# Performance work log

Hardware: AMD Instinct MI355X
Metric: run time of the kernel (lower is better)

Reference implementation:

```python
import jax, jax.numpy as jnp
import numpy as np
import math

N = 20000          # nodes (residues)
E = 640000         # edges
CS = 384           # c_s
CZ = 128           # c_z
CH = 16            # c_hidden
H = 8              # no_heads
PQK = 8            # no_qk_points == no_v_points (forced equal, see notes)
FS = 128           # scalar channels in feat_irreps
PIN = 16           # vector channels in feat_irreps
HC = H * CH        # 128
HPQ = H * PQK * 3  # 192
CZ4 = CZ // 4      # 32
OUT_IN = HC + 3 * H + H + H * CZ4  # 416 actual concat width
INF = 100000.0
EPS = 1e-8


def setup_inputs() -> dict:
    key = jax.random.key(0)
    ks = jax.random.split(key, 16)
    w = lambda k, i, o: (jax.random.normal(k, (i, o), jnp.float32) / np.float32(np.sqrt(i)))
    frame_s = jax.random.normal(ks[0], (N, CS), jnp.float32)
    tfn_t = jax.random.normal(ks[1], (N, FS + 3 * PIN), jnp.float32)
    z = jax.random.normal(ks[2], (E, CZ), jnp.float32)
    edge_index = jax.random.randint(ks[3], (2, E), 0, N)
    mask = jnp.ones((N,), jnp.float32)
    # Rigid transforms: proper-ish rotations via QR, translations
    rot, _ = jnp.linalg.qr(jax.random.normal(ks[4], (N, 3, 3), jnp.float32))
    trans = jax.random.normal(ks[5], (N, 3), jnp.float32)
    return {
        "frame_s": frame_s, "tfn_t": tfn_t, "z": z,
        "edge_index": edge_index, "mask": mask,
        "rot": rot, "trans": trans,
        "Wq": w(ks[6], CS, HC), "bq": jnp.zeros((HC,), jnp.float32),
        "Wk_s": w(ks[7], FS, HC), "Wk_v": w(ks[8], PIN, PQK),
        "Wqp": w(ks[9], CS, HPQ), "bqp": jnp.zeros((HPQ,), jnp.float32),
        "Wb": w(ks[10], CZ, H), "bb": jnp.zeros((H,), jnp.float32),
        "Wdz": w(ks[11], CZ, CZ4), "bdz": jnp.zeros((CZ4,), jnp.float32),
        # ipa_point_weights_init_: softplus(hw) == 1  =>  hw = log(e - 1)
        "head_weights": jnp.full((H,), np.float32(np.log(np.e - 1.0))),
        "Wout": w(ks[12], OUT_IN, CS), "bout": jnp.zeros((CS,), jnp.float32),
    }


def _segment_softmax(a, seg, n):
    # pyg-style numerically stable segment softmax over edges grouped by seg
    m = jax.ops.segment_max(a, seg, num_segments=n)
    m = jnp.where(jnp.isfinite(m), m, 0.0)
    e = jnp.exp(a - m[seg])
    s = jax.ops.segment_sum(e, seg, num_segments=n)
    return e / (s[seg] + 1e-16)


def _forward(frame_s, tfn_t, z, mask, rot, trans,
             Wq, bq, Wk_s, Wk_v, Wqp, bqp, Wb, bb, Wdz, bdz,
             head_weights, Wout, bout, edge_index):
    n = frame_s.shape[0]
    src = edge_index[1]
    dst = edge_index[0]

    # scalar queries: [N,H,C]
    q = (frame_s @ Wq + bq).reshape(n, H, CH)

    # o3.Linear (feat_irreps -> k_irreps): scalars mix scalars, vectors mix vectors.
    # NOTE: original code uses linear_k for BOTH k and v (faithful bug), so v==k.
    scal = tfn_t[:, :FS]
    vecs = tfn_t[:, FS:].reshape(n, PIN, 3)
    k_scal = scal @ Wk_s                                   # [N, HC]
    k_vec = jnp.einsum('npx,pq->nqx', vecs, Wk_v)          # [N, PQK, 3]
    k = k_scal.reshape(n, H, CH)
    v = k
    k_tail = k_vec.reshape(n, PQK * 3)                     # [N, 24]
    # torch: split([3]*PQK) then stack(dim=-1) -> [N,3,PQK], then view [N,H,-1,3]
    k_pts = jnp.stack(jnp.split(k_tail, PQK, axis=-1), axis=-1)  # [N,3,PQK]
    k_pts = k_pts.reshape(n, H, -1, 3)                     # [N,H,1,3]
    v_pts = k_pts

    # query points, rigid-transformed: [N,H,PQK,3]
    q_pts = frame_s @ Wqp + bqp                            # [N, 3*H*PQK]
    q_pts = jnp.stack(jnp.split(q_pts, 3, axis=-1), axis=-1)  # [N, H*PQK, 3]
    q_pts = jnp.einsum('nij,npj->npi', rot, q_pts) + trans[:, None, :]
    q_pts = q_pts.reshape(n, H, PQK, 3)

    # scalar attention logits [E,H]
    a = jnp.einsum('ehc,ehc->eh', q[src], k[dst])
    a = a * np.float32(math.sqrt(1.0 / (3 * CH)))
    b = z @ Wb + bb                                        # [E,H]
    a = a + np.float32(math.sqrt(1.0 / 3)) * b

    # point attention: disp [E,H,PQK,3] (k_pts broadcasts over points)
    disp = q_pts[src] - k_pts[dst]
    pt_att = jnp.sum(disp * disp, axis=-1)                 # [E,H,PQK]
    hw = jax.nn.softplus(head_weights) * np.float32(math.sqrt(1.0 / (3 * (PQK * 9.0 / 2))))
    pt_att = -0.5 * jnp.sum(pt_att * hw[None, :, None], axis=-1)  # [E,H]

    edge_mask = INF * (mask[dst] * mask[src] - 1.0)        # [E]
    a = a + pt_att + edge_mask[:, None]

    a = _segment_softmax(a, src, n)                        # [E,H]

    # scalar output
    o = jax.ops.segment_sum(a[..., None] * v[dst], src, num_segments=n)  # [N,H,C]
    o = o.reshape(n, HC)

    # point output
    o_pt = jax.ops.segment_sum(a[:, :, None, None] * v_pts[dst], src, num_segments=n)  # [N,H,1,3]
    o_pt = jnp.einsum('nji,nhpj->nhpi', rot, o_pt - trans[:, None, None, :])  # invert_apply
    o_pt_norm = jnp.sqrt(jnp.sum(o_pt * o_pt, axis=-1) + EPS).reshape(n, H)
    o_pt = o_pt.reshape(n, -1, 3)                          # [N,H,3]

    # pair output
    pair_z = z @ Wdz + bdz                                 # [E,CZ4]
    o_pair = jax.ops.segment_sum(a[..., None] * pair_z[:, None, :], src, num_segments=n)  # [N,H,CZ4]
    o_pair = o_pair.reshape(n, H * CZ4)

    feats = jnp.concatenate(
        [o, o_pt[..., 0], o_pt[..., 1], o_pt[..., 2], o_pt_norm, o_pair], axis=-1)  # [N,416]
    return feats @ Wout + bout                             # [N, CS]


def reference(frame_s, tfn_t, z, edge_index, mask, rot, trans,
              Wq, bq, Wk_s, Wk_v, Wqp, bqp, Wb, bb, Wdz, bdz,
              head_weights, Wout, bout):
    return _forward(frame_s, tfn_t, z, mask, rot, trans,
                    Wq, bq, Wk_s, Wk_v, Wqp, bqp, Wb, bb, Wdz, bdz,
                    head_weights, Wout, bout, edge_index)
```

## Files before the change

### kernel.cpp

```cpp
#include <hip/hip_runtime.h>
#include <math.h>

typedef __attribute__((ext_vector_type(8))) short short8;
typedef __attribute__((ext_vector_type(4))) float f32x4;

static __device__ inline unsigned short f2bf(float f) {
    union { float f; unsigned u; } v; v.f = f;
    unsigned r = v.u + 0x7FFF + ((v.u >> 16) & 1);
    return (unsigned short)(r >> 16);
}

template<int WJ>
__global__ __launch_bounds__(256) void gemm_mfma(
    const float* __restrict__ A, int lda,
    const float* __restrict__ BT, int ldb,
    const float* __restrict__ bias,
    float* __restrict__ C, int ldc,
    int M, int N, int K)
{
    constexpr int GBN = WJ * 32;
    __shared__ unsigned short As[128 * 72];
    __shared__ unsigned short Bs[GBN * 72];

    const int t = threadIdx.x;
    const int wid = t >> 6, lane = t & 63;
    const int wm = (wid & 1) * 64;
    const int wn = (wid >> 1) * (WJ * 16);
    const int row16 = lane & 15, quad = lane >> 4;
    const int bm = blockIdx.x * 128;
    const int bn = blockIdx.y * GBN;

    f32x4 acc[4][WJ];
    #pragma unroll
    for (int i = 0; i < 4; ++i)
        #pragma unroll
        for (int j = 0; j < WJ; ++j)
            #pragma unroll
            for (int r = 0; r < 4; ++r) acc[i][j][r] = 0.f;

    const int ktiles = (K + 63) >> 6;
    for (int kt = 0; kt < ktiles; ++kt) {
        const int k0 = kt << 6;
        #pragma unroll
        for (int it = 0; it < 8; ++it) {
            int f = it * 256 + t;
            int row = f >> 4, kq = (f & 15) << 2;
            float4 av = make_float4(0.f, 0.f, 0.f, 0.f);
            if (bm + row < M && k0 + kq < K)
                av = *(const float4*)(A + (size_t)(bm + row) * lda + k0 + kq);
            ushort4 uv;
            uv.x = f2bf(av.x); uv.y = f2bf(av.y); uv.z = f2bf(av.z); uv.w = f2bf(av.w);
            *(ushort4*)(&As[row * 72 + kq]) = uv;
        }
        #pragma unroll
        for (int it = 0; it < WJ * 2; ++it) {
            int f = it * 256 + t;
            int row = f >> 4, kq = (f & 15) << 2;
            float4 bv = make_float4(0.f, 0.f, 0.f, 0.f);
            if (bn + row < N && k0 + kq < K)
                bv = *(const float4*)(BT + (size_t)(bn + row) * ldb + k0 + kq);
            ushort4 uv;
            uv.x = f2bf(bv.x); uv.y = f2bf(bv.y); uv.z = f2bf(bv.z); uv.w = f2bf(bv.w);
            *(ushort4*)(&Bs[row * 72 + kq]) = uv;
        }
        __syncthreads();

        #pragma unroll
        for (int ks = 0; ks < 64; ks += 32) {
            short8 af[4], bfv[WJ];
            #pragma unroll
            for (int i = 0; i < 4; ++i)
                af[i] = *(const short8*)(&As[(wm + i * 16 + row16) * 72 + ks + quad * 8]);
            #pragma unroll
            for (int j = 0; j < WJ; ++j)
                bfv[j] = *(const short8*)(&Bs[(wn + j * 16 + row16) * 72 + ks + quad * 8]);
            #pragma unroll
            for (int i = 0; i < 4; ++i)
                #pragma unroll
                for (int j = 0; j < WJ; ++j)
                    acc[i][j] = __builtin_amdgcn_mfma_f32_16x16x32_bf16(af[i], bfv[j], acc[i][j], 0, 0, 0);
        }
        __syncthreads();
    }

    #pragma unroll
    for (int i = 0; i < 4; ++i)
        #pragma unroll
        for (int j = 0; j < WJ; ++j) {
            int col = bn + wn + j * 16 + row16;
            if (col >= N) continue;
            float bv = bias ? bias[col] : 0.f;
            #pragma unroll
            for (int r = 0; r < 4; ++r) {
                int row = bm + wm + i * 16 + quad * 4 + r;
                if (row < M) C[(size_t)row * ldc + col] = acc[i][j][r] + bv;
            }
        }
}

__global__ void prep_kernel(const float* __restrict__ Wq, const float* __restrict__ bq,
                            const float* __restrict__ Wqp, const float* __restrict__ bqp,
                            const float* __restrict__ Wb, const float* __restrict__ bb,
                            const float* __restrict__ Wdz, const float* __restrict__ bdz,
                            const float* __restrict__ Wks, const float* __restrict__ Wout,
                            float* __restrict__ wqqpT, float* __restrict__ bqqp,
                            float* __restrict__ wcatT, float* __restrict__ bcat,
                            float* __restrict__ wksT, float* __restrict__ woutT)
{
    int gid = blockIdx.x * 256 + threadIdx.x;
    int stride = gridDim.x * 256;
    for (int i = gid; i < 320 * 384; i += stride) {
        int o = i / 384, c = i % 384;
        wqqpT[i] = (o < 128) ? Wq[c * 128 + o] : Wqp[c * 192 + (o - 128)];
    }
    for (int i = gid; i < 320; i += stride) bqqp[i] = (i < 128) ? bq[i] : bqp[i - 128];
    for (int i = gid; i < 40 * 128; i += stride) {
        int o = i >> 7, c = i & 127;
        wcatT[i] = (o < 8) ? Wb[c * 8 + o] : Wdz[c * 32 + (o - 8)];
    }
    for (int i = gid; i < 40; i += stride) bcat[i] = (i < 8) ? bb[i] : bdz[i - 8];
    for (int i = gid; i < 128 * 128; i += stride) {
        int o = i >> 7, c = i & 127;
        wksT[i] = Wks[c * 128 + o];
    }
    for (int i = gid; i < 384 * 416; i += stride) {
        int o = i / 416, c = i % 416;
        woutT[i] = Wout[c * 384 + o];
    }
}

__global__ void kpts_kernel(const float* __restrict__ tfn, const float* __restrict__ Wkv,
                            float* __restrict__ kpts, int n)
{
    int t = blockIdx.x * 256 + threadIdx.x;
    if (t >= n * 24) return;
    int node = t / 24, f = t % 24;
    int a = f >> 3;
    int b = f & 7;
    const float* vr = tfn + (size_t)node * 176 + 128;
    float s = 0.f;
    #pragma unroll
    for (int p = 0; p < 16; ++p) s += vr[p * 3 + a] * Wkv[p * 8 + b];
    kpts[t] = s;
}

__global__ void qpts_kernel(const float* __restrict__ qpraw, const float* __restrict__ rot,
                            const float* __restrict__ trans, float* __restrict__ qpts, int n)
{
    int t = blockIdx.x * 256 + threadIdx.x;
    if (t >= n * 64) return;
    int node = t / 64, hk = t % 64;
    const float* qr = qpraw + (size_t)node * 320;
    float r0 = qr[hk], r1 = qr[64 + hk], r2 = qr[128 + hk];
    const float* R = rot + (size_t)node * 9;
    const float* T = trans + (size_t)node * 3;
    float* o = qpts + (size_t)node * 192 + hk * 3;
    #pragma unroll
    for (int i = 0; i < 3; ++i)
        o[i] = R[i * 3 + 0] * r0 + R[i * 3 + 1] * r1 + R[i * 3 + 2] * r2 + T[i];
}

__global__ void count_kernel(const int* __restrict__ srcA, int* __restrict__ cnt, int E)
{
    int e = blockIdx.x * 256 + threadIdx.x;
    if (e < E) atomicAdd(&cnt[srcA[e]], 1);
}

__global__ void scan_kernel(const int* __restrict__ cnt, int* __restrict__ off,
                            int* __restrict__ cur, int n)
{
    __shared__ int sums[1024];
    int t = threadIdx.x;
    int chunk = (n + 1023) >> 10;
    int begin = t * chunk;
    int local = 0;
    for (int j = 0; j < chunk; ++j) {
        int i = begin + j;
        if (i < n) local += cnt[i];
    }
    sums[t] = local;
    __syncthreads();
    for (int d = 1; d < 1024; d <<= 1) {
        int x = sums[t];
        int y = (t >= d) ? sums[t - d] : 0;
        __syncthreads();
        sums[t] = x + y;
        __syncthreads();
    }
    int run = sums[t] - local;
    for (int j = 0; j < chunk; ++j) {
        int i = begin + j;
        if (i < n) {
            off[i] = run;
            cur[i] = run;
            run += cnt[i];
        }
    }
}

__global__ void fill_kernel(const int* __restrict__ srcA, int* __restrict__ cur,
                            int* __restrict__ elist, int E)
{
    int e = blockIdx.x * 256 + threadIdx.x;
    if (e < E) {
        int s = srcA[e];
        int pos = atomicAdd(&cur[s], 1);
        elist[pos] = e;
    }
}

__global__ __launch_bounds__(256) void attn_kernel(
    const int* __restrict__ dstA,
    const int* __restrict__ off, const int* __restrict__ cnt, const int* __restrict__ elist,
    const float* __restrict__ qqp, const float* __restrict__ kbuf,
    const float* __restrict__ qpts, const float* __restrict__ kpts,
    const float* __restrict__ bpair, const float* __restrict__ mask,
    const float* __restrict__ hwin,
    const float* __restrict__ rot, const float* __restrict__ trans,
    float* __restrict__ feats, int n)
{
    int wave = threadIdx.x >> 6;
    int lane = threadIdx.x & 63;
    int s = blockIdx.x * 4 + wave;
    if (s >= n) return;
    int es = lane >> 3;
    int h  = lane & 7;

    float qh[16];
    {
        const float* qp = qqp + (size_t)s * 320 + h * 16;
        #pragma unroll
        for (int c = 0; c < 16; ++c) qh[c] = qp[c];
    }
    float qpt[24];
    {
        const float* pp = qpts + (size_t)s * 192 + h * 24;
        #pragma unroll
        for (int j = 0; j < 24; ++j) qpt[j] = pp[j];
    }
    float hwv = log1pf(__expf(hwin[h])) * 0.09622504486493764f;
    float mask_s = mask[s];
    int myoff = off[s], mycnt = cnt[s];

    float ssum = 0.f;
    float oacc[16];
    #pragma unroll
    for (int c = 0; c < 16; ++c) oacc[c] = 0.f;
    float optacc[3] = {0.f, 0.f, 0.f};
    float opacc[8][4];
    #pragma unroll
    for (int j = 0; j < 8; ++j)
        #pragma unroll
        for (int c = 0; c < 4; ++c) opacc[j][c] = 0.f;

    int nb = (mycnt + 7) >> 3;
    for (int b = 0; b < nb; ++b) {
        int idx = b * 8 + es;
        bool valid = idx < mycnt;
        int e = valid ? elist[myoff + idx] : 0;
        int d = dstA[e];

        const float* kr = kbuf + (size_t)d * 128 + h * 16;
        float4 ka = *(const float4*)(kr + 0);
        float4 kb = *(const float4*)(kr + 4);
        float4 kc = *(const float4*)(kr + 8);
        float4 kd = *(const float4*)(kr + 12);

        const float* kp = kpts + (size_t)d * 24 + h * 3;
        float kp0 = kp[0], kp1 = kp[1], kp2 = kp[2];

        const float* bp = bpair + (size_t)e * 40;
        float bh = bp[h];
        float4 pair4 = *(const float4*)(bp + 8 + h * 4);

        float qk = qh[0] * ka.x + qh[1] * ka.y + qh[2] * ka.z + qh[3] * ka.w
                 + qh[4] * kb.x + qh[5] * kb.y + qh[6] * kb.z + qh[7] * kb.w
                 + qh[8] * kc.x + qh[9] * kc.y + qh[10] * kc.z + qh[11] * kc.w
                 + qh[12] * kd.x + qh[13] * kd.y + qh[14] * kd.z + qh[15] * kd.w;

        float pt = 0.f;
        #pragma unroll
        for (int pp = 0; pp < 8; ++pp) {
            float d0 = qpt[pp * 3 + 0] - kp0;
            float d1 = qpt[pp * 3 + 1] - kp1;
            float d2 = qpt[pp * 3 + 2] - kp2;
            pt += d0 * d0 + d1 * d1 + d2 * d2;
        }

        float md = mask[d];
        float logit = 0.14433756729740643f * qk
                    + 0.5773502691896258f * bh
                    - 0.5f * hwv * pt
                    + 100000.0f * (mask_s * md - 1.0f);
        float w = valid ? __expf(logit) : 0.f;

        ssum += w;
        oacc[0] += w * ka.x; oacc[1] += w * ka.y; oacc[2] += w * ka.z; oacc[3] += w * ka.w;
        oacc[4] += w * kb.x; oacc[5] += w * kb.y; oacc[6] += w * kb.z; oacc[7] += w * kb.w;
        oacc[8] += w * kc.x; oacc[9] += w * kc.y; oacc[10] += w * kc.z; oacc[11] += w * kc.w;
        oacc[12] += w * kd.x; oacc[13] += w * kd.y; oacc[14] += w * kd.z; oacc[15] += w * kd.w;
        optacc[0] += w * kp0;
        optacc[1] += w * kp1;
        optacc[2] += w * kp2;

        #pragma unroll
        for (int jh = 0; jh < 8; ++jh) {
            float wj = __shfl(w, (es << 3) + jh);
            opacc[jh][0] += wj * pair4.x;
            opacc[jh][1] += wj * pair4.y;
            opacc[jh][2] += wj * pair4.z;
            opacc[jh][3] += wj * pair4.w;
        }
    }

    #pragma unroll
    for (int delta = 8; delta <= 32; delta <<= 1) {
        ssum += __shfl_xor(ssum, delta);
        #pragma unroll
        for (int c = 0; c < 16; ++c) oacc[c] += __shfl_xor(oacc[c], delta);
        #pragma unroll
        for (int i = 0; i < 3; ++i) optacc[i] += __shfl_xor(optacc[i], delta);
        #pragma unroll
        for (int j = 0; j < 8; ++j)
            #pragma unroll
            for (int c = 0; c < 4; ++c) opacc[j][c] += __shfl_xor(opacc[j][c], delta);
    }

    float invj[8];
    #pragma unroll
    for (int jh = 0; jh < 8; ++jh)
        invj[jh] = 1.f / (__shfl(ssum, jh) + 1e-16f);

    if (es == 0) {
        float inv = 1.f / (ssum + 1e-16f);
        float* f = feats + (size_t)s * 416;
        #pragma unroll
        for (int c = 0; c < 16; c += 4) {
            float4 v = make_float4(oacc[c] * inv, oacc[c + 1] * inv, oacc[c + 2] * inv, oacc[c + 3] * inv);
            *(float4*)(&f[h * 16 + c]) = v;
        }
        const float* T = trans + (size_t)s * 3;
        const float* R = rot + (size_t)s * 9;
        float v0 = optacc[0] * inv - T[0];
        float v1 = optacc[1] * inv - T[1];
        float v2 = optacc[2] * inv - T[2];
        float r0 = R[0] * v0 + R[3] * v1 + R[6] * v2;
        float r1 = R[1] * v0 + R[4] * v1 + R[7] * v2;
        float r2 = R[2] * v0 + R[5] * v1 + R[8] * v2;
        f[128 + h] = r0;
        f[136 + h] = r1;
        f[144 + h] = r2;
        f[152 + h] = sqrtf(r0 * r0 + r1 * r1 + r2 * r2 + 1e-8f);
        #pragma unroll
        for (int jh = 0; jh < 8; ++jh) {
            float4 v = make_float4(opacc[jh][0] * invj[jh], opacc[jh][1] * invj[jh],
                                   opacc[jh][2] * invj[jh], opacc[jh][3] * invj[jh]);
            *(float4*)(&f[160 + jh * 32 + h * 4]) = v;
        }
    }
}

extern "C" void kernel_launch(void* const* d_in, const int* in_sizes, int n_in,
                              void* d_out, int out_size, void* d_ws, size_t ws_size,
                              hipStream_t stream)
{
    const float* frame_s = (const float*)d_in[0];
    const float* tfn     = (const float*)d_in[1];
    const float* z       = (const float*)d_in[2];
    const int*   ei      = (const int*)d_in[3];
    const float* mask    = (const float*)d_in[4];
    const float* rot     = (const float*)d_in[5];
    const float* trans   = (const float*)d_in[6];
    const float* Wq      = (const float*)d_in[7];
    const float* bq      = (const float*)d_in[8];
    const float* Wks     = (const float*)d_in[9];
    const float* Wkv     = (const float*)d_in[10];
    const float* Wqp     = (const float*)d_in[11];
    const float* bqp     = (const float*)d_in[12];
    const float* Wb      = (const float*)d_in[13];
    const float* bb      = (const float*)d_in[14];
    const float* Wdz     = (const float*)d_in[15];
    const float* bdz     = (const float*)d_in[16];
    const float* hw      = (const float*)d_in[17];
    const float* Wout    = (const float*)d_in[18];
    const float* bout    = (const float*)d_in[19];
    float* out = (float*)d_out;

    int n = in_sizes[0] / 384;
    int E = in_sizes[3] / 2;
    const int* dstA = ei;
    const int* srcA = ei + E;

    float* ws = (float*)d_ws;
    size_t p = 0;
    auto alloc = [&](size_t elems) -> float* {
        float* r = ws + p;
        p += (elems + 15) & ~((size_t)15);
        return r;
    };
    float* qqpbuf = alloc((size_t)n * 320);
    float* qpts   = alloc((size_t)n * 192);
    float* kbuf   = alloc((size_t)n * 128);
    float* kpts   = alloc((size_t)n * 24);
    float* feats  = alloc((size_t)n * 416);
    float* bpair  = alloc((size_t)E * 40);
    float* wqqpT  = alloc(320 * 384);
    float* bqqp   = alloc(320);
    float* wcatT  = alloc(40 * 128);
    float* bcat   = alloc(64);
    float* wksT   = alloc(128 * 128);
    float* woutT  = alloc(384 * 416);
    int* cnt   = (int*)alloc((size_t)n);
    int* off   = (int*)alloc((size_t)n);
    int* cur   = (int*)alloc((size_t)n);
    int* elist = (int*)alloc((size_t)E);

    hipMemsetAsync(cnt, 0, (size_t)n * sizeof(int), stream);
    prep_kernel<<<512, 256, 0, stream>>>(Wq, bq, Wqp, bqp, Wb, bb, Wdz, bdz, Wks, Wout,
                                         wqqpT, bqqp, wcatT, bcat, wksT, woutT);

    count_kernel<<<(E + 255) / 256, 256, 0, stream>>>(srcA, cnt, E);
    scan_kernel<<<1, 1024, 0, stream>>>(cnt, off, cur, n);
    fill_kernel<<<(E + 255) / 256, 256, 0, stream>>>(srcA, cur, elist, E);

    {
        dim3 g((n + 127) / 128, (320 + 127) / 128);
        gemm_mfma<4><<<g, 256, 0, stream>>>(frame_s, 384, wqqpT, 384, bqqp, qqpbuf, 320, n, 320, 384);
    }
    {
        dim3 g((n + 127) / 128, 1);
        gemm_mfma<4><<<g, 256, 0, stream>>>(tfn, 176, wksT, 128, nullptr, kbuf, 128, n, 128, 128);
    }
    {
        dim3 g((E + 127) / 128, 1);
        gemm_mfma<2><<<g, 256, 0, stream>>>(z, 128, wcatT, 128, bcat, bpair, 40, E, 40, 128);
    }
    kpts_kernel<<<(n * 24 + 255) / 256, 256, 0, stream>>>(tfn, Wkv, kpts, n);
    qpts_kernel<<<(n * 64 + 255) / 256, 256, 0, stream>>>(qqpbuf + 128, rot, trans, qpts, n);

    attn_kernel<<<(n + 3) / 4, 256, 0, stream>>>(dstA, off, cnt, elist,
                                                 qqpbuf, kbuf, qpts, kpts, bpair, mask, hw,
                                                 rot, trans, feats, n);

    {
        dim3 g((n + 127) / 128, (384 + 127) / 128);
        gemm_mfma<4><<<g, 256, 0, stream>>>(feats, 416, woutT, 416, bout, out, 384, n, 384, 416);
    }
    (void)n_in; (void)out_size; (void)ws_size;
}
```

Baseline: 905.6 us.

## Gather edge GEMM into CSR order, fold logit scales into weights, widen GEMM tiles

Measured after the change: 966.7 us. 1.07x slower.

```diff
diff --git a/kernel.cpp b/kernel.cpp
--- a/kernel.cpp
+++ b/kernel.cpp
@@ -10,9 +10,10 @@
     return (unsigned short)(r >> 16);
 }
 
-template<int WJ>
+template<int WJ, bool GATHER>
 __global__ __launch_bounds__(256) void gemm_mfma(
     const float* __restrict__ A, int lda,
+    const int* __restrict__ gidx,
     const float* __restrict__ BT, int ldb,
     const float* __restrict__ bias,
     float* __restrict__ C, int ldc,
@@ -46,8 +47,12 @@
             int f = it * 256 + t;
             int row = f >> 4, kq = (f & 15) << 2;
             float4 av = make_float4(0.f, 0.f, 0.f, 0.f);
-            if (bm + row < M && k0 + kq < K)
-                av = *(const float4*)(A + (size_t)(bm + row) * lda + k0 + kq);
+            if (bm + row < M && k0 + kq < K) {
+                size_t ar;
+                if constexpr (GATHER) ar = (size_t)gidx[bm + row];
+                else                  ar = (size_t)(bm + row);
+                av = *(const float4*)(A + ar * lda + k0 + kq);
+            }
             ushort4 uv;
             uv.x = f2bf(av.x); uv.y = f2bf(av.y); uv.z = f2bf(av.z); uv.w = f2bf(av.w);
             *(ushort4*)(&As[row * 72 + kq]) = uv;
@@ -105,20 +110,24 @@
                             const float* __restrict__ Wks, const float* __restrict__ Wout,
                             float* __restrict__ wqqpT, float* __restrict__ bqqp,
                             float* __restrict__ wcatT, float* __restrict__ bcat,
-                            float* __restrict__ wksT, float* __restrict__ woutT)
-{
+                            float* __restrict__ wksT, float* __restrict__ woutT,
+                            int* __restrict__ cnt, int n)
+{
+    const float SC_QK = 0.14433756729740643f;
+    const float SC_B  = 0.5773502691896258f;
     int gid = blockIdx.x * 256 + threadIdx.x;
     int stride = gridDim.x * 256;
+    for (int i = gid; i < n; i += stride) cnt[i] = 0;
     for (int i = gid; i < 320 * 384; i += stride) {
         int o = i / 384, c = i % 384;
-        wqqpT[i] = (o < 128) ? Wq[c * 128 + o] : Wqp[c * 192 + (o - 128)];
-    }
-    for (int i = gid; i < 320; i += stride) bqqp[i] = (i < 128) ? bq[i] : bqp[i - 128];
+        wqqpT[i] = (o < 128) ? Wq[c * 128 + o] * SC_QK : Wqp[c * 192 + (o - 128)];
+    }
+    for (int i = gid; i < 320; i += stride) bqqp[i] = (i < 128) ? bq[i] * SC_QK : bqp[i - 128];
     for (int i = gid; i < 40 * 128; i += stride) {
         int o = i >> 7, c = i & 127;
-        wcatT[i] = (o < 8) ? Wb[c * 8 + o] : Wdz[c * 32 + (o - 8)];
-    }
-    for (int i = gid; i < 40; i += stride) bcat[i] = (i < 8) ? bb[i] : bdz[i - 8];
+        wcatT[i] = (o < 8) ? Wb[c * 8 + o] * SC_B : Wdz[c * 32 + (o - 8)];
+    }
+    for (int i = gid; i < 40; i += stride) bcat[i] = (i < 8) ? bb[i] * SC_B : bdz[i - 8];
     for (int i = gid; i < 128 * 128; i += stride) {
         int o = i >> 7, c = i & 127;
         wksT[i] = Wks[c * 128 + o];
@@ -198,20 +207,22 @@
     }
 }
 
-__global__ void fill_kernel(const int* __restrict__ srcA, int* __restrict__ cur,
-                            int* __restrict__ elist, int E)
+__global__ void fill_kernel(const int* __restrict__ srcA, const int* __restrict__ dstA,
+                            int* __restrict__ cur, int* __restrict__ elist,
+                            int* __restrict__ dsts, int E)
 {
     int e = blockIdx.x * 256 + threadIdx.x;
     if (e < E) {
         int s = srcA[e];
         int pos = atomicAdd(&cur[s], 1);
         elist[pos] = e;
+        dsts[pos] = dstA[e];
     }
 }
 
 __global__ __launch_bounds__(256) void attn_kernel(
-    const int* __restrict__ dstA,
-    const int* __restrict__ off, const int* __restrict__ cnt, const int* __restrict__ elist,
+    const int* __restrict__ off, const int* __restrict__ cnt,
+    const int* __restrict__ dsts,
     const float* __restrict__ qqp, const float* __restrict__ kbuf,
     const float* __restrict__ qpts, const float* __restrict__ kpts,
     const float* __restrict__ bpair, const float* __restrict__ mask,
@@ -238,7 +249,7 @@
         #pragma unroll
         for (int j = 0; j < 24; ++j) qpt[j] = pp[j];
     }
-    float hwv = log1pf(__expf(hwin[h])) * 0.09622504486493764f;
+    float hwv = log1pf(__expf(hwin[h])) * 0.04811252243246882f;
     float mask_s = mask[s];
     int myoff = off[s], mycnt = cnt[s];
 
@@ -257,8 +268,12 @@
     for (int b = 0; b < nb; ++b) {
         int idx = b * 8 + es;
         bool valid = idx < mycnt;
-        int e = valid ? elist[myoff + idx] : 0;
-        int d = dstA[e];
+        int pos = myoff + (valid ? idx : 0);
+        int d = dsts[pos];
+
+        const float* bp = bpair + (size_t)pos * 40;
+        float bh = bp[h];
+        float4 pair4 = *(const float4*)(bp + 8 + h * 4);
 
         const float* kr = kbuf + (size_t)d * 128 + h * 16;
         float4 ka = *(const float4*)(kr + 0);
@@ -269,10 +284,6 @@
         const float* kp = kpts + (size_t)d * 24 + h * 3;
         float kp0 = kp[0], kp1 = kp[1], kp2 = kp[2];
 
-        const float* bp = bpair + (size_t)e * 40;
-        float bh = bp[h];
-        float4 pair4 = *(const float4*)(bp + 8 + h * 4);
-
         float qk = qh[0] * ka.x + qh[1] * ka.y + qh[2] * ka.z + qh[3] * ka.w
                  + qh[4] * kb.x + qh[5] * kb.y + qh[6] * kb.z + qh[7] * kb.w
                  + qh[8] * kc.x + qh[9] * kc.y + qh[10] * kc.z + qh[11] * kc.w
@@ -288,10 +299,7 @@
         }
 
         float md = mask[d];
-        float logit = 0.14433756729740643f * qk
-                    + 0.5773502691896258f * bh
-                    - 0.5f * hwv * pt
-                    + 100000.0f * (mask_s * md - 1.0f);
+        float logit = qk + bh - hwv * pt + 100000.0f * (mask_s * md - 1.0f);
         float w = valid ? __expf(logit) : 0.f;
 
         ssum += w;
@@ -414,37 +422,37 @@
     int* off   = (int*)alloc((size_t)n);
     int* cur   = (int*)alloc((size_t)n);
     int* elist = (int*)alloc((size_t)E);
-
-    hipMemsetAsync(cnt, 0, (size_t)n * sizeof(int), stream);
+    int* dsts  = (int*)alloc((size_t)E);
+
     prep_kernel<<<512, 256, 0, stream>>>(Wq, bq, Wqp, bqp, Wb, bb, Wdz, bdz, Wks, Wout,
-                                         wqqpT, bqqp, wcatT, bcat, wksT, woutT);
+                                         wqqpT, bqqp, wcatT, bcat, wksT, woutT, cnt, n);
 
     count_kernel<<<(E + 255) / 256, 256, 0, stream>>>(srcA, cnt, E);
     scan_kernel<<<1, 1024, 0, stream>>>(cnt, off, cur, n);
-    fill_kernel<<<(E + 255) / 256, 256, 0, stream>>>(srcA, cur, elist, E);
-
-    {
-        dim3 g((n + 127) / 128, (320 + 127) / 128);
-        gemm_mfma<4><<<g, 256, 0, stream>>>(frame_s, 384, wqqpT, 384, bqqp, qqpbuf, 320, n, 320, 384);
+    fill_kernel<<<(E + 255) / 256, 256, 0, stream>>>(srcA, dstA, cur, elist, dsts, E);
+
+    {
+        dim3 g((n + 127) / 128, 2);
+        gemm_mfma<5, false><<<g, 256, 0, stream>>>(frame_s, 384, nullptr, wqqpT, 384, bqqp, qqpbuf, 320, n, 320, 384);
     }
     {
         dim3 g((n + 127) / 128, 1);
-        gemm_mfma<4><<<g, 256, 0, stream>>>(tfn, 176, wksT, 128, nullptr, kbuf, 128, n, 128, 128);
+        gemm_mfma<4, false><<<g, 256, 0, stream>>>(tfn, 176, nullptr, wksT, 128, nullptr, kbuf, 128, n, 128, 128);
     }
     {
         dim3 g((E + 127) / 128, 1);
-        gemm_mfma<2><<<g, 256, 0, stream>>>(z, 128, wcatT, 128, bcat, bpair, 40, E, 40, 128);
+        gemm_mfma<2, true><<<g, 256, 0, stream>>>(z, 128, elist, wcatT, 128, bcat, bpair, 40, E, 40, 128);
     }
     kpts_kernel<<<(n * 24 + 255) / 256, 256, 0, stream>>>(tfn, Wkv, kpts, n);
     qpts_kernel<<<(n * 64 + 255) / 256, 256, 0, stream>>>(qqpbuf + 128, rot, trans, qpts, n);
 
-    attn_kernel<<<(n + 3) / 4, 256, 0, stream>>>(dstA, off, cnt, elist,
+    attn_kernel<<<(n + 3) / 4, 256, 0, stream>>>(off, cnt, dsts,
                                                  qqpbuf, kbuf, qpts, kpts, bpair, mask, hw,
                                                  rot, trans, feats, n);
 
     {
-        dim3 g((n + 127) / 128, (384 + 127) / 128);
-        gemm_mfma<4><<<g, 256, 0, stream>>>(feats, 416, woutT, 416, bout, out, 384, n, 384, 416);
+        dim3 g((n + 127) / 128, 2);
+        gemm_mfma<6, false><<<g, 256, 0, stream>>>(feats, 416, nullptr, woutT, 416, bout, out, 384, n, 384, 416);
     }
     (void)n_in; (void)out_size; (void)ws_size;
 }
```
